# Optimization experiments

Measured on AMD Instinct MI355X. Metric: run time of the kernel, lower is better.

Reference implementation:

```python
import jax, jax.numpy as jnp
import numpy as np

BS, C, D = 4096, 16384, 128
POS_ALPHA, POS_DELTA = 32.0, 0.1
NEG_ALPHA, NEG_DELTA = 32.0, -0.1


def _normalize(x):
    # F.normalize(x, dim=1)
    return x / jnp.linalg.norm(x, axis=1, keepdims=True)


def _masked_lse(sims, mask, axis, use_max):
    """Faithful port of Criterion.masked_logsumexp (returns per-entry lse and the
    nonzero-entry mask that torch uses to filter before the final mean)."""
    m = sims * mask
    if use_max:
        ref = jnp.max(m, axis=axis, keepdims=True)
    else:
        ref = jnp.min(m, axis=axis, keepdims=True)
    ref = jax.lax.stop_gradient(ref)  # torch: ref_v.detach()
    # torch: nz_entries = max + min of (sims*mask); keep where nonzero
    nz = (jnp.max(m, axis=axis) + jnp.min(m, axis=axis)) != 0
    s = jnp.sum(jnp.exp(sims - ref) * mask, axis=axis)
    lse = jnp.log(jnp.where(nz, s, 1.0)) + jnp.squeeze(ref, axis=axis)
    return lse, nz


def setup_inputs() -> dict:
    key = jax.random.key(0)
    k1, k2, k3 = jax.random.split(key, 3)
    batch = jax.random.normal(k1, (BS, D), dtype=jnp.float32)
    # proxies = randn/proxy_div, init_dev=0 so no max-shift
    proxies = jax.random.normal(k2, (C, D), dtype=jnp.float32) / 8.0
    labels = jax.random.randint(k3, (BS,), 0, C)
    return {"batch": batch, "proxies": proxies, "labels": labels}


def reference(batch, proxies, labels):
    batch = _normalize(batch)          # [BS, D]
    proxies = _normalize(proxies)      # [C, D]

    pos_sims = batch @ proxies[labels].T   # [BS, BS] cosine sims to positive proxies
    sims = batch @ proxies.T               # [BS, C]

    same = (labels[:, None] == labels[None, :]).astype(batch.dtype)              # [BS, BS]
    diff = (labels[:, None] != jnp.arange(C)[None, :]).astype(batch.dtype)       # [BS, C]

    w_pos = -POS_ALPHA * (pos_sims - POS_DELTA)
    w_neg = NEG_ALPHA * (sims - NEG_DELTA)

    # mode='anchor' -> dim=0; cosine -> max=False for pos, max=True for neg
    pos_lse, pos_nz = _masked_lse(w_pos, same, axis=0, use_max=False)
    neg_lse, neg_nz = _masked_lse(w_neg, diff, axis=0, use_max=True)

    # nca_clean=False -> softplus
    pos_s = jax.nn.softplus(pos_lse)
    neg_s = jax.nn.softplus(neg_lse)

    # torch takes mean only over nz entries
    pos_mean = jnp.sum(jnp.where(pos_nz, pos_s, 0.0)) / jnp.maximum(jnp.sum(pos_nz), 1).astype(batch.dtype)
    neg_mean = jnp.sum(jnp.where(neg_nz, neg_s, 0.0)) / jnp.maximum(jnp.sum(neg_nz), 1).astype(batch.dtype)
    return pos_mean + neg_mean
```

## Files before the change

kernel.cpp:

```cpp
#include <hip/hip_runtime.h>
#include <math.h>

#define BS 4096
#define C_CLS 16384
#define D 128
#define NS 8
#define NR 8
#define KE 46.16624130844683f
#define POS_C 4.616624130844683f
#define LN2 0.69314718055994531f
#define CORR_BLOCKS 256
#define NEG_BLOCKS 512

typedef __attribute__((ext_vector_type(8))) short short8;
typedef __attribute__((ext_vector_type(4))) float f32x4;

__device__ inline float bf2f(unsigned short h) {
    return __uint_as_float(((unsigned)h) << 16);
}
__device__ inline unsigned short f2bf(float f) {
    unsigned u = __float_as_uint(f);
    u += 0x7FFF + ((u >> 16) & 1);
    return (unsigned short)(u >> 16);
}
__device__ inline float fastexp2(float x) {
    return __int_as_float((int)fmaf(x, 8388608.0f, 1064866816.0f));
}
__device__ inline float softplus(float x) {
    return fmaxf(x, 0.0f) + log1pf(__expf(-fabsf(x)));
}
__device__ inline void gload16(const void* g, void* l) {
    __builtin_amdgcn_global_load_lds((const __attribute__((address_space(1))) void*)g,
                                     (__attribute__((address_space(3))) void*)l, 16, 0, 0);
}
__device__ inline unsigned fenc(float f) {
    unsigned u = __float_as_uint(f);
    return (u & 0x80000000u) ? ~u : (u | 0x80000000u);
}
__device__ inline float fdec(unsigned k) {
    return (k & 0x80000000u) ? __uint_as_float(k ^ 0x80000000u) : __uint_as_float(~k);
}

__global__ __launch_bounds__(256) void normalize_all(const float* __restrict__ batch,
                                                     const float* __restrict__ proxies,
                                                     short* __restrict__ bbf,
                                                     short* __restrict__ pbf,
                                                     float* __restrict__ acc,
                                                     float* __restrict__ negSub,
                                                     float* __restrict__ posSum,
                                                     float* __restrict__ posCnt,
                                                     unsigned* __restrict__ posMaxK,
                                                     unsigned* __restrict__ posMinK,
                                                     int* __restrict__ counter) {
    const int sub = threadIdx.x >> 5;
    const int lane32 = threadIdx.x & 31;
    const int row = blockIdx.x * 8 + sub;
    const bool isb = row < BS;
    const float* src = isb ? batch : proxies;
    short* dst = isb ? bbf : pbf;
    const int r = isb ? row : row - BS;
    const float sc = isb ? 1.0f : KE;

    float4 v = ((const float4*)(src + (size_t)r * D))[lane32];
    float ss = v.x * v.x + v.y * v.y + v.z * v.z + v.w * v.w;
#pragma unroll
    for (int off = 16; off; off >>= 1) ss += __shfl_xor(ss, off);
    float inv = rsqrtf(ss) * sc;
    ushort4 o;
    o.x = f2bf(v.x * inv);
    o.y = f2bf(v.y * inv);
    o.z = f2bf(v.z * inv);
    o.w = f2bf(v.w * inv);
    ((ushort4*)(dst + (size_t)r * D))[lane32] = o;

    const int bid = blockIdx.x, t = threadIdx.x;
    if (bid < 64) negSub[bid * 256 + t] = 0.0f;
    else if (bid < 128) posSum[(bid - 64) * 256 + t] = 0.0f;
    else if (bid < 192) posCnt[(bid - 128) * 256 + t] = 0.0f;
    else if (bid < 256) posMaxK[(bid - 192) * 256 + t] = 0u;
    else if (bid < 320) posMinK[(bid - 256) * 256 + t] = 0xFFFFFFFFu;
    if (bid == 0 && t == 0) *counter = 0;
}

__global__ __launch_bounds__(256, 1) void mm_all(const short* __restrict__ pbf,
                                                 const short* __restrict__ bbf,
                                                 const int* __restrict__ labels,
                                                 float* __restrict__ S,
                                                 float* __restrict__ negSub,
                                                 float* __restrict__ posSum,
                                                 float* __restrict__ posCnt,
                                                 unsigned* __restrict__ posMaxK,
                                                 unsigned* __restrict__ posMinK) {
    __shared__ short8 frag[2][16 * 64];

    const int bid = blockIdx.x;
    const int tid = threadIdx.x;
    const int w = tid >> 6, lane = tid & 63, l16 = lane & 15, g = lane >> 4;

    if (bid < CORR_BLOCKS) {
        const int ibase = bid * 16 + w * 4;
        int lab[4];
        float d[4];
#pragma unroll
        for (int r = 0; r < 4; r++) {
            const int i = ibase + r;
            lab[r] = labels[i];
            ushort2 av = ((const ushort2*)(bbf + (size_t)i * D))[lane];
            ushort2 pv = ((const ushort2*)(pbf + (size_t)lab[r] * D))[lane];
            d[r] = bf2f(av.x) * bf2f(pv.x) + bf2f(av.y) * bf2f(pv.y);
        }
#pragma unroll
        for (int off = 32; off; off >>= 1)
#pragma unroll
            for (int r = 0; r < 4; r++) d[r] += __shfl_xor(d[r], off);

        if (lane == 0) {
#pragma unroll
            for (int r = 0; r < 4; r++) {
                atomicAdd(&negSub[lab[r]], fastexp2(d[r]));
                atomicAdd(&posSum[lab[r]], fastexp2(POS_C - d[r]));
                atomicAdd(&posCnt[lab[r]], 1.0f);
                unsigned k = fenc(fmaf(d[r], -LN2, 3.2f));
                atomicMax(&posMaxK[lab[r]], k);
                atomicMin(&posMinK[lab[r]], k);
            }
        }
        return;
    }

    const int n = bid - CORR_BLOCKS;
    const int pg = (n & 7) * 8 + ((n >> 3) & 7);
    const int sp = n >> 6;
    const int wbase = pg * 256 + w * 64;

    short8 a[4][4];
#pragma unroll
    for (int pt = 0; pt < 4; pt++)
#pragma unroll
        for (int kk = 0; kk < 4; kk++)
            a[pt][kk] = *(const short8*)(pbf + (size_t)(wbase + pt * 16 + l16) * D + kk * 32 + g * 8);
#pragma unroll
    for (int pt = 0; pt < 4; pt++)
#pragma unroll
        for (int kk = 0; kk < 4; kk++)
            asm volatile("" : "+v"(a[pt][kk]));

    float s[4][4];
#pragma unroll
    for (int pt = 0; pt < 4; pt++)
#pragma unroll
        for (int r = 0; r < 4; r++) s[pt][r] = 0.0f;

    const int ibeg = sp * (BS / NS);
    const short* srcbase = bbf + (size_t)(ibeg + w * 16 + l16) * D + g * 8;

#define STAGE(rr)                                                            \
    {                                                                        \
        const short* sn_ = srcbase + (size_t)(rr) * 64 * D;                  \
        _Pragma("unroll") for (int kk = 0; kk < 4; kk++)                     \
            gload16(sn_ + kk * 32, &frag[(rr) & 1][(w * 4 + kk) * 64]);      \
    }

    STAGE(0)
    asm volatile("s_waitcnt vmcnt(0)" ::: "memory");
    __syncthreads();

    for (int rnd = 0; rnd < NR; rnd++) {
        const int cur = rnd & 1;
        if (rnd + 1 < NR) STAGE(rnd + 1)

        const short8* fb = &frag[cur][0];
#pragma unroll
        for (int bt = 0; bt < 4; bt++) {
            short8 b[4];
#pragma unroll
            for (int kk = 0; kk < 4; kk++) b[kk] = fb[(bt * 4 + kk) * 64 + lane];
#pragma unroll
            for (int pt = 0; pt < 4; pt++) {
                f32x4 acc = {0.0f, 0.0f, 0.0f, 0.0f};
#pragma unroll
                for (int kk = 0; kk < 4; kk++)
                    acc = __builtin_amdgcn_mfma_f32_16x16x32_bf16(a[pt][kk], b[kk], acc, 0, 0, 0);
#pragma unroll
                for (int r = 0; r < 4; r++) s[pt][r] += fastexp2(acc[r]);
            }
        }
        asm volatile("s_waitcnt vmcnt(0)" ::: "memory");
        __syncthreads();
    }
#undef STAGE

#pragma unroll
    for (int off = 1; off < 16; off <<= 1)
#pragma unroll
        for (int pt = 0; pt < 4; pt++)
#pragma unroll
            for (int r = 0; r < 4; r++) s[pt][r] += __shfl_xor(s[pt][r], off);

    if (l16 == 0) {
#pragma unroll
        for (int pt = 0; pt < 4; pt++)
#pragma unroll
            for (int r = 0; r < 4; r++) {
                int row = wbase + pt * 16 + g * 4 + r;
                S[(size_t)sp * C_CLS + row] = s[pt][r];
            }
    }
}

__global__ __launch_bounds__(256) void final_reduce(const float* __restrict__ S,
                                                    const float* __restrict__ negSub,
                                                    const int* __restrict__ labels,
                                                    const float* __restrict__ posSum,
                                                    const float* __restrict__ posCnt,
                                                    const unsigned* __restrict__ posMaxK,
                                                    const unsigned* __restrict__ posMinK,
                                                    float* __restrict__ acc,
                                                    int* __restrict__ counter,
                                                    float* __restrict__ out) {
    const int n = blockIdx.x * 256 + threadIdx.x;
    float add = 0.0f, cnt = 0.0f;
    int slot;
    if (n < C_CLS) {
        slot = 2;
        float s = 0.0f;
#pragma unroll
        for (int p = 0; p < NS; p++) s += S[(size_t)p * C_CLS + n];
        s = fmaxf(s - negSub[n], 1e-30f);
        add = softplus(logf(s) + 3.2f);
        cnt = 1.0f;
    } else {
        slot = 0;
        const int j = n - C_CLS;
        const int lab = labels[j];
        float s = posSum[lab], c = posCnt[lab];
        float mxw = fdec(posMaxK[lab]), mnw = fdec(posMinK[lab]);
        float maxm = (c < (float)BS) ? fmaxf(mxw, 0.0f) : mxw;
        float minm = (c < (float)BS) ? fminf(mnw, 0.0f) : mnw;
        bool nz = (maxm + minm) != 0.0f;
        if (nz) {
            add = softplus(logf(s));
            cnt = 1.0f;
        }
    }
#pragma unroll
    for (int off = 32; off; off >>= 1) {
        add += __shfl_xor(add, off);
        cnt += __shfl_xor(cnt, off);
    }
    if ((threadIdx.x & 63) == 0) {
        atomicAdd(&acc[slot], add);
        atomicAdd(&acc[slot + 1], cnt);
    }

    __shared__ int amLast;
    __threadfence();
    if (threadIdx.x == 0) amLast = (atomicAdd(counter, 1) == (int)gridDim.x - 1);
    __syncthreads();
    if (amLast && threadIdx.x == 0) {
        __threadfence();
        out[0] = acc[0] / fmaxf(acc[1], 1.0f) + acc[2] / fmaxf(acc[3], 1.0f);
    }
}

extern "C" void kernel_launch(void* const* d_in, const int* in_sizes, int n_in,
                              void* d_out, int out_size, void* d_ws, size_t ws_size,
                              hipStream_t stream) {
    const float* batch = (const float*)d_in[0];
    const float* proxies = (const float*)d_in[1];
    const int* labels = (const int*)d_in[2];
    float* out = (float*)d_out;

    char* ws = (char*)d_ws;
    float* acc = (float*)ws;
    int* counter = (int*)(ws + 64);
    short* bbf = (short*)(ws + 256);
    short* pbf = (short*)(ws + 256 + (size_t)BS * D * 2);
    char* p = ws + 256 + (size_t)(BS + C_CLS) * D * 2;
    float* negS = (float*)p;          p += (size_t)C_CLS * NS * 4;
    float* negSub = (float*)p;        p += (size_t)C_CLS * 4;
    float* posSum = (float*)p;        p += (size_t)C_CLS * 4;
    float* posCnt = (float*)p;        p += (size_t)C_CLS * 4;
    unsigned* posMaxK = (unsigned*)p; p += (size_t)C_CLS * 4;
    unsigned* posMinK = (unsigned*)p;

    normalize_all<<<(BS + C_CLS) / 8, 256, 0, stream>>>(batch, proxies, bbf, pbf, acc,
                                                        negSub, posSum, posCnt, posMaxK,
                                                        posMinK, counter);
    mm_all<<<CORR_BLOCKS + NEG_BLOCKS, 256, 0, stream>>>(pbf, bbf, labels, negS, negSub,
                                                         posSum, posCnt, posMaxK, posMinK);
    final_reduce<<<(C_CLS + BS) / 256, 256, 0, stream>>>(negS, negSub, labels, posSum,
                                                         posCnt, posMaxK, posMinK,
                                                         acc, counter, out);
}
```

Before: 45.68 us.

## Give each wave private LDS buffers and pipeline batch chunks without block barriers

The cooperative block-wide LDS staging with __syncthreads per round is replaced by per-wave double-buffered LDS chunks of 16 batch rows. Each wave loads its own chunk with a two-deep prefetch and uses vmcnt waits instead of barriers, and it issues all MFMAs before the exp accumulation. The launch bound no longer forces one block per CU, which may allow higher occupancy. The cost is that every wave now loads the same batch rows separately, so redundant global traffic rises fourfold per block.

```diff
diff --git a/kernel.cpp b/kernel.cpp
--- a/kernel.cpp
+++ b/kernel.cpp
@@ -5,7 +5,7 @@
 #define C_CLS 16384
 #define D 128
 #define NS 8
-#define NR 8
+#define NCH 32
 #define KE 46.16624130844683f
 #define POS_C 4.616624130844683f
 #define LN2 0.69314718055994531f
@@ -82,16 +82,16 @@
     if (bid == 0 && t == 0) *counter = 0;
 }
 
-__global__ __launch_bounds__(256, 1) void mm_all(const short* __restrict__ pbf,
-                                                 const short* __restrict__ bbf,
-                                                 const int* __restrict__ labels,
-                                                 float* __restrict__ S,
-                                                 float* __restrict__ negSub,
-                                                 float* __restrict__ posSum,
-                                                 float* __restrict__ posCnt,
-                                                 unsigned* __restrict__ posMaxK,
-                                                 unsigned* __restrict__ posMinK) {
-    __shared__ short8 frag[2][16 * 64];
+__global__ __launch_bounds__(256) void mm_all(const short* __restrict__ pbf,
+                                              const short* __restrict__ bbf,
+                                              const int* __restrict__ labels,
+                                              float* __restrict__ S,
+                                              float* __restrict__ negSub,
+                                              float* __restrict__ posSum,
+                                              float* __restrict__ posCnt,
+                                              unsigned* __restrict__ posMaxK,
+                                              unsigned* __restrict__ posMinK) {
+    __shared__ short8 lds[4][2][4 * 64];
 
     const int bid = blockIdx.x;
     const int tid = threadIdx.x;
@@ -152,41 +152,46 @@
         for (int r = 0; r < 4; r++) s[pt][r] = 0.0f;
 
     const int ibeg = sp * (BS / NS);
-    const short* srcbase = bbf + (size_t)(ibeg + w * 16 + l16) * D + g * 8;
-
-#define STAGE(rr)                                                            \
-    {                                                                        \
-        const short* sn_ = srcbase + (size_t)(rr) * 64 * D;                  \
-        _Pragma("unroll") for (int kk = 0; kk < 4; kk++)                     \
-            gload16(sn_ + kk * 32, &frag[(rr) & 1][(w * 4 + kk) * 64]);      \
+    const short* srcbase = bbf + (size_t)(ibeg + l16) * D + g * 8;
+    short8* myl = &lds[w][0][0];
+
+#define STAGE(cc)                                                             \
+    {                                                                         \
+        const short* sn_ = srcbase + (size_t)(cc) * 16 * D;                   \
+        _Pragma("unroll") for (int kk = 0; kk < 4; kk++)                      \
+            gload16(sn_ + kk * 32, &myl[((cc) & 1) * 256 + kk * 64]);         \
     }
 
     STAGE(0)
-    asm volatile("s_waitcnt vmcnt(0)" ::: "memory");
-    __syncthreads();
-
-    for (int rnd = 0; rnd < NR; rnd++) {
-        const int cur = rnd & 1;
-        if (rnd + 1 < NR) STAGE(rnd + 1)
-
-        const short8* fb = &frag[cur][0];
-#pragma unroll
-        for (int bt = 0; bt < 4; bt++) {
-            short8 b[4];
-#pragma unroll
-            for (int kk = 0; kk < 4; kk++) b[kk] = fb[(bt * 4 + kk) * 64 + lane];
-#pragma unroll
-            for (int pt = 0; pt < 4; pt++) {
-                f32x4 acc = {0.0f, 0.0f, 0.0f, 0.0f};
-#pragma unroll
-                for (int kk = 0; kk < 4; kk++)
-                    acc = __builtin_amdgcn_mfma_f32_16x16x32_bf16(a[pt][kk], b[kk], acc, 0, 0, 0);
-#pragma unroll
-                for (int r = 0; r < 4; r++) s[pt][r] += fastexp2(acc[r]);
-            }
+    STAGE(1)
+
+    for (int c = 0; c < NCH; c++) {
+        if (c < NCH - 1)
+            asm volatile("s_waitcnt vmcnt(4)" ::: "memory");
+        else
+            asm volatile("s_waitcnt vmcnt(0)" ::: "memory");
+
+        const short8* fb = &myl[(c & 1) * 256];
+        short8 b[4];
+#pragma unroll
+        for (int kk = 0; kk < 4; kk++) b[kk] = fb[kk * 64 + lane];
+
+        f32x4 acc[4];
+#pragma unroll
+        for (int pt = 0; pt < 4; pt++) {
+            acc[pt] = (f32x4){0.0f, 0.0f, 0.0f, 0.0f};
+#pragma unroll
+            for (int kk = 0; kk < 4; kk++)
+                acc[pt] = __builtin_amdgcn_mfma_f32_16x16x32_bf16(a[pt][kk], b[kk], acc[pt], 0, 0, 0);
         }
-        asm volatile("s_waitcnt vmcnt(0)" ::: "memory");
-        __syncthreads();
+
+        asm volatile("s_waitcnt lgkmcnt(0)" ::: "memory");
+        if (c + 2 < NCH) STAGE(c + 2)
+
+#pragma unroll
+        for (int pt = 0; pt < 4; pt++)
+#pragma unroll
+            for (int r = 0; r < 4; r++) s[pt][r] += fastexp2(acc[pt][r]);
     }
 #undef STAGE
 
```

Result: slower. 58.06 us (+27.1%).
